# Kernel tuning notes

Hardware: AMD Instinct MI355X
Metric: run time of the kernel (lower is better)

Reference implementation:

```python
import jax, jax.numpy as jnp
import numpy as np

N_NODES = 100000
N_EDGES = 640000
IN_FEATS = 256
HEADS = 4
OUT_FEATS = 32
NEG_SLOPE = 0.2


def setup_inputs() -> dict:
    key = jax.random.key(0)
    k_feat, k_src, k_dst, k_w, k_al, k_ar = jax.random.split(key, 6)
    feat = jax.random.normal(k_feat, (N_NODES, IN_FEATS), dtype=jnp.float32)
    src = jax.random.randint(k_src, (N_EDGES,), 0, N_NODES, dtype=jnp.int32)
    dst = jax.random.randint(k_dst, (N_EDGES,), 0, N_NODES, dtype=jnp.int32)
    # fc: Linear(in_feats, out_feats*num_heads, bias=False); store as [in, H*D]
    W = jax.random.normal(k_w, (IN_FEATS, HEADS * OUT_FEATS), dtype=jnp.float32) * 0.05
    attn_l = jax.random.normal(k_al, (HEADS, OUT_FEATS), dtype=jnp.float32) * 0.1
    attn_r = jax.random.normal(k_ar, (HEADS, OUT_FEATS), dtype=jnp.float32) * 0.1
    return {"feat": feat, "W": W, "attn_l": attn_l, "attn_r": attn_r, "src": src, "dst": dst}


def reference(feat, W, attn_l, attn_r, src, dst):
    N = feat.shape[0]
    H, D = attn_l.shape
    # fc + reshape to [N, H, D]
    ft = (feat @ W).reshape(N, H, D)
    # per-node attention logits [N, H]
    el = jnp.einsum('nhd,hd->nh', ft, attn_l)
    er = jnp.einsum('nhd,hd->nh', ft, attn_r)
    # u_add_v then leaky relu -> per-edge logits [E, H]
    e = el[src] + er[dst]
    e = jnp.where(e > 0, e, NEG_SLOPE * e)
    # edge softmax over incoming edges of each dst node (per head)
    m = jax.ops.segment_max(e, dst, num_segments=N)  # [N, H]
    m = jnp.where(jnp.isfinite(m), m, jnp.zeros_like(m))  # empty segments
    ex = jnp.exp(e - m[dst])
    denom = jax.ops.segment_sum(ex, dst, num_segments=N)  # [N, H]
    a = ex / denom[dst]  # [E, H]
    # u_mul_e + sum aggregation: rst[v] = sum_{(u,v)} a_uv * ft[u]
    msg = ft[src] * a[:, :, None]  # [E, H, D]
    rst = jax.ops.segment_sum(msg, dst, num_segments=N)  # [N, H, D]
    return rst, a[:, :, None]
```

## Files before the change

kernel.cpp:

```cpp
#include <hip/hip_runtime.h>
#include <hip/hip_bf16.h>

#define N_NODES 100000
#define N_EDGES 640000
#define IN_F 256
#define HD 128

using f32x4 = __attribute__((ext_vector_type(4))) float;
using s8v   = __attribute__((ext_vector_type(8))) short;

__device__ __forceinline__ short bf16h(float x) {
  __hip_bfloat16 h = __float2bfloat16(x);
  return (short)__builtin_bit_cast(unsigned short, h);
}
__device__ __forceinline__ float bf16tof(short h) {
  unsigned u = ((unsigned)(unsigned short)h) << 16;
  return __builtin_bit_cast(float, u);
}

__global__ __launch_bounds__(256) void prep_b(const float* __restrict__ W,
                                              short* __restrict__ Bth)
{
  int c = blockIdx.x;
  int k = threadIdx.x;
  Bth[(size_t)c * IN_F + k] = bf16h(W[(size_t)k * HD + c]);
}

__global__ __launch_bounds__(256) void prep_x(const float* __restrict__ W,
    const float* __restrict__ al, const float* __restrict__ ar,
    short* __restrict__ Bxh)
{
  int c = blockIdx.x;
  int k = threadIdx.x;
  float v = 0.f;
  if (c < 8) {
    int h = c & 3;
    const float* att = (c < 4) ? al : ar;
    #pragma unroll
    for (int d = 0; d < 32; d++)
      v += W[(size_t)k * HD + h * 32 + d] * att[h * 32 + d];
  }
  Bxh[(size_t)c * IN_F + k] = bf16h(v);
}

__global__ __launch_bounds__(256) void gemm_mfma(const float* __restrict__ feat,
    const short* __restrict__ Bth, const short* __restrict__ Bxh,
    float* __restrict__ ft, float* __restrict__ el, float* __restrict__ er, int M)
{
  const int wid  = threadIdx.x >> 6;
  const int lane = threadIdx.x & 63;
  const int lr = lane & 15;
  const int lg = lane >> 4;
  const int wm = (wid >> 1) * 32;
  const int wn = (wid & 1) * 64;
  const int rb = blockIdx.x * 64;
  const bool doX = (wid & 1) == 0;

  f32x4 acc[2][4];
  f32x4 accx[2];
  #pragma unroll
  for (int mi = 0; mi < 2; mi++) {
    accx[mi] = (f32x4){0.f, 0.f, 0.f, 0.f};
    #pragma unroll
    for (int ni = 0; ni < 4; ni++) acc[mi][ni] = (f32x4){0.f, 0.f, 0.f, 0.f};
  }

  const float* ap[2];
  #pragma unroll
  for (int mi = 0; mi < 2; mi++) {
    int r = rb + wm + mi * 16 + lr;
    if (r > M - 1) r = M - 1;
    ap[mi] = feat + (size_t)r * IN_F + lg * 8;
  }
  const short* bp[4];
  #pragma unroll
  for (int ni = 0; ni < 4; ni++)
    bp[ni] = Bth + (size_t)(wn + ni * 16 + lr) * IN_F + lg * 8;
  const short* xp = Bxh + (size_t)lr * IN_F + lg * 8;

  float4 A0[3][2], A1[3][2];
  s8v Bb[2][4], Xb[2];

  #pragma unroll
  for (int mi = 0; mi < 2; mi++) {
    A0[0][mi] = *(const float4*)(ap[mi]);       A1[0][mi] = *(const float4*)(ap[mi] + 4);
    A0[1][mi] = *(const float4*)(ap[mi] + 32);  A1[1][mi] = *(const float4*)(ap[mi] + 36);
  }
  #pragma unroll
  for (int ni = 0; ni < 4; ni++) Bb[0][ni] = *(const s8v*)(bp[ni]);
  Xb[0] = *(const s8v*)xp;

  #pragma unroll
  for (int kt = 0; kt < 8; ++kt) {
    const int cur = kt % 3, pre = (kt + 2) % 3;
    const int curb = kt & 1, preb = curb ^ 1;
    if (kt + 2 < 8) {
      #pragma unroll
      for (int mi = 0; mi < 2; mi++) {
        A0[pre][mi] = *(const float4*)(ap[mi] + (kt + 2) * 32);
        A1[pre][mi] = *(const float4*)(ap[mi] + (kt + 2) * 32 + 4);
      }
    }
    if (kt + 1 < 8) {
      #pragma unroll
      for (int ni = 0; ni < 4; ni++) Bb[preb][ni] = *(const s8v*)(bp[ni] + (kt + 1) * 32);
      Xb[preb] = *(const s8v*)(xp + (kt + 1) * 32);
    }
    #pragma unroll
    for (int mi = 0; mi < 2; mi++) {
      const float av[8] = {A0[cur][mi].x, A0[cur][mi].y, A0[cur][mi].z, A0[cur][mi].w,
                           A1[cur][mi].x, A1[cur][mi].y, A1[cur][mi].z, A1[cur][mi].w};
      s8v ah, alo;
      #pragma unroll
      for (int j = 0; j < 8; j++) {
        short h = bf16h(av[j]);
        ah[j]  = h;
        alo[j] = bf16h(av[j] - bf16tof(h));
      }
      #pragma unroll
      for (int ni = 0; ni < 4; ni++) {
        acc[mi][ni] = __builtin_amdgcn_mfma_f32_16x16x32_bf16(ah,  Bb[curb][ni], acc[mi][ni], 0, 0, 0);
        acc[mi][ni] = __builtin_amdgcn_mfma_f32_16x16x32_bf16(alo, Bb[curb][ni], acc[mi][ni], 0, 0, 0);
      }
      if (doX) {
        accx[mi] = __builtin_amdgcn_mfma_f32_16x16x32_bf16(ah,  Xb[curb], accx[mi], 0, 0, 0);
        accx[mi] = __builtin_amdgcn_mfma_f32_16x16x32_bf16(alo, Xb[curb], accx[mi], 0, 0, 0);
      }
    }
  }

  #pragma unroll
  for (int mi = 0; mi < 2; mi++) {
    int rbase = rb + wm + mi * 16 + lg * 4;
    #pragma unroll
    for (int ni = 0; ni < 4; ni++) {
      int col = wn + ni * 16 + lr;
      #pragma unroll
      for (int r = 0; r < 4; r++) {
        int grow = rbase + r;
        if (grow < M) ft[(size_t)grow * HD + col] = acc[mi][ni][r];
      }
    }
    if (doX) {
      #pragma unroll
      for (int r = 0; r < 4; r++) {
        int grow = rbase + r;
        if (grow < M) {
          if (lr < 4)      el[(size_t)grow * 4 + lr]       = accx[mi][r];
          else if (lr < 8) er[(size_t)grow * 4 + (lr - 4)] = accx[mi][r];
        }
      }
    }
  }
}

__global__ void deg_kernel(const int* __restrict__ dst, int* __restrict__ deg) {
  int i = blockIdx.x * blockDim.x + threadIdx.x;
  if (i < N_EDGES) atomicAdd(&deg[dst[i]], 1);
}

__global__ __launch_bounds__(256) void scanA(const int* __restrict__ deg,
    int* __restrict__ excl, int* __restrict__ partials, int n)
{
  __shared__ int s[256];
  int t = threadIdx.x;
  int base = blockIdx.x * 1024 + t * 4;
  int d0 = (base + 0 < n) ? deg[base + 0] : 0;
  int d1 = (base + 1 < n) ? deg[base + 1] : 0;
  int d2 = (base + 2 < n) ? deg[base + 2] : 0;
  int d3 = (base + 3 < n) ? deg[base + 3] : 0;
  int sum = d0 + d1 + d2 + d3;
  s[t] = sum; __syncthreads();
  for (int off = 1; off < 256; off <<= 1) {
    int x = 0; if (t >= off) x = s[t - off];
    __syncthreads(); s[t] += x; __syncthreads();
  }
  int e0 = s[t] - sum;
  if (base + 0 < n) excl[base + 0] = e0;
  if (base + 1 < n) excl[base + 1] = e0 + d0;
  if (base + 2 < n) excl[base + 2] = e0 + d0 + d1;
  if (base + 3 < n) excl[base + 3] = e0 + d0 + d1 + d2;
  if (t == 255) partials[blockIdx.x] = s[255];
}

__global__ void scanB(int* partials, int nb) {
  __shared__ int s[128];
  int t = threadIdx.x;
  int v = (t < nb) ? partials[t] : 0;
  s[t] = v; __syncthreads();
  for (int off = 1; off < 128; off <<= 1) {
    int x = 0; if (t >= off) x = s[t - off];
    __syncthreads(); s[t] += x; __syncthreads();
  }
  if (t < nb) partials[t] = s[t] - v;
}

__global__ __launch_bounds__(256) void scanC(int* __restrict__ row_ptr,
    const int* __restrict__ partials, int n, int E)
{
  int t = threadIdx.x;
  int base = blockIdx.x * 1024 + t * 4;
  int add = partials[blockIdx.x];
  #pragma unroll
  for (int j = 0; j < 4; j++) if (base + j < n) row_ptr[base + j] += add;
  if (blockIdx.x == 0 && t == 0) row_ptr[n] = E;
}

__global__ void scatter_kernel(const int* __restrict__ src, const int* __restrict__ dst,
                               const int* __restrict__ row_ptr,
                               int* __restrict__ cursor, int* __restrict__ usrc) {
  int e = blockIdx.x * blockDim.x + threadIdx.x;
  if (e >= N_EDGES) return;
  int d = dst[e];
  int pos = row_ptr[d] + atomicAdd(&cursor[d], 1);
  usrc[pos] = src[e];
}

__global__ __launch_bounds__(256) void gat_node(const int* __restrict__ row_ptr,
    const int* __restrict__ usrc,
    const float* __restrict__ el, const float* __restrict__ er4,
    const float* __restrict__ ft, float* __restrict__ rst,
    float* __restrict__ lse, int n)
{
  __shared__ int   su[4][64];
  __shared__ float sex[4][64][4];
  const int w = threadIdx.x >> 6;
  const int lane = threadIdx.x & 63;
  const int v = blockIdx.x * 4 + w;
  if (v >= n) return;
  const int s0 = row_ptr[v];
  const int d  = row_ptr[v + 1] - s0;
  const int g  = lane >> 4;

  if (d == 0) {
    *(float2*)(rst + (size_t)v * HD + 2 * lane) = make_float2(0.f, 0.f);
    return;
  }

  const float4 erv = *(const float4*)(er4 + (size_t)v * 4);
  float m0 = -1e30f, m1 = -1e30f, m2 = -1e30f, m3 = -1e30f;
  float den = 0.f;
  float2 acc = make_float2(0.f, 0.f);

  for (int c0 = 0; c0 < d; c0 += 64) {
    const int cd = min(64, d - c0);
    float x0 = -1e30f, x1 = -1e30f, x2 = -1e30f, x3 = -1e30f;
    int u = 0;
    if (lane < cd) {
      u = usrc[s0 + c0 + lane];
      const float4 elv = *(const float4*)(el + (size_t)u * 4);
      x0 = elv.x + erv.x; x0 = x0 > 0.f ? x0 : 0.2f * x0;
      x1 = elv.y + erv.y; x1 = x1 > 0.f ? x1 : 0.2f * x1;
      x2 = elv.z + erv.z; x2 = x2 > 0.f ? x2 : 0.2f * x2;
      x3 = elv.w + erv.w; x3 = x3 > 0.f ? x3 : 0.2f * x3;
    }
    su[w][lane] = u;
    float n0 = x0, n1 = x1, n2 = x2, n3 = x3;
    #pragma unroll
    for (int off = 32; off >= 1; off >>= 1) {
      n0 = fmaxf(n0, __shfl_xor(n0, off));
      n1 = fmaxf(n1, __shfl_xor(n1, off));
      n2 = fmaxf(n2, __shfl_xor(n2, off));
      n3 = fmaxf(n3, __shfl_xor(n3, off));
    }
    n0 = fmaxf(n0, m0); n1 = fmaxf(n1, m1); n2 = fmaxf(n2, m2); n3 = fmaxf(n3, m3);
    float e0 = __expf(x0 - n0), e1 = __expf(x1 - n1);
    float e2 = __expf(x2 - n2), e3 = __expf(x3 - n3);
    sex[w][lane][0] = e0; sex[w][lane][1] = e1;
    sex[w][lane][2] = e2; sex[w][lane][3] = e3;
    float mg = g == 0 ? m0 : g == 1 ? m1 : g == 2 ? m2 : m3;
    float ng = g == 0 ? n0 : g == 1 ? n1 : g == 2 ? n2 : n3;
    float scale = __expf(mg - ng);
    den *= scale; acc.x *= scale; acc.y *= scale;
    m0 = n0; m1 = n1; m2 = n2; m3 = n3;
    asm volatile("s_waitcnt lgkmcnt(0)" ::: "memory");
    #pragma unroll 4
    for (int j = 0; j < cd; ++j) {
      int uu = su[w][j];
      float wgt = sex[w][j][g];
      float2 f = *(const float2*)(ft + (size_t)uu * HD + 2 * lane);
      den += wgt;
      acc.x += wgt * f.x; acc.y += wgt * f.y;
    }
  }
  *(float2*)(rst + (size_t)v * HD + 2 * lane) = make_float2(acc.x / den, acc.y / den);
  if ((lane & 15) == 0) {
    float mg = g == 0 ? m0 : g == 1 ? m1 : g == 2 ? m2 : m3;
    lse[(size_t)v * 4 + g] = mg + __logf(den);
  }
}

__global__ void norm_kernel(const int* __restrict__ src, const int* __restrict__ dst,
                            const float* __restrict__ el, const float* __restrict__ er,
                            const float* __restrict__ lse, float* __restrict__ a, int E)
{
  int i = blockIdx.x * blockDim.x + threadIdx.x;
  if (i >= E) return;
  int u = src[i], v = dst[i];
  const float4 elv = *(const float4*)(el + (size_t)u * 4);
  const float4 erv = *(const float4*)(er + (size_t)v * 4);
  const float4 ls  = *(const float4*)(lse + (size_t)v * 4);
  float x0 = elv.x + erv.x; x0 = x0 > 0.f ? x0 : 0.2f * x0;
  float x1 = elv.y + erv.y; x1 = x1 > 0.f ? x1 : 0.2f * x1;
  float x2 = elv.z + erv.z; x2 = x2 > 0.f ? x2 : 0.2f * x2;
  float x3 = elv.w + erv.w; x3 = x3 > 0.f ? x3 : 0.2f * x3;
  float4 o;
  o.x = __expf(x0 - ls.x); o.y = __expf(x1 - ls.y);
  o.z = __expf(x2 - ls.z); o.w = __expf(x3 - ls.w);
  *(float4*)(a + (size_t)i * 4) = o;
}

extern "C" void kernel_launch(void* const* d_in, const int* in_sizes, int n_in,
                              void* d_out, int out_size, void* d_ws, size_t ws_size,
                              hipStream_t stream)
{
  const float* feat = (const float*)d_in[0];
  const float* W    = (const float*)d_in[1];
  const float* al   = (const float*)d_in[2];
  const float* ar   = (const float*)d_in[3];
  const int*   src  = (const int*)d_in[4];
  const int*   dst  = (const int*)d_in[5];
  float* rst   = (float*)d_out;
  float* a_out = rst + (size_t)N_NODES * HD;

  char* w = (char*)d_ws;
  auto alloc = [&](size_t bytes) { char* p = w; w += (bytes + 255) & ~(size_t)255; return p; };
  float* ft      = (float*)alloc((size_t)N_NODES * HD * 4);
  float* el      = (float*)alloc((size_t)N_NODES * 4 * 4);
  float* er      = (float*)alloc((size_t)N_NODES * 4 * 4);
  float* lse     = (float*)alloc((size_t)N_NODES * 4 * 4);
  int*   deg     = (int*)alloc((size_t)N_NODES * 4);
  int*   row_ptr = (int*)alloc(((size_t)N_NODES + 1) * 4);
  int*   cursor  = (int*)alloc((size_t)N_NODES * 4);
  int*   partials= (int*)alloc(1024);
  int*   usrc    = (int*)alloc((size_t)N_EDGES * 4);
  short* Bth     = (short*)alloc((size_t)HD * IN_F * 2);
  short* Bxh     = (short*)alloc((size_t)16 * IN_F * 2);

  hipMemsetAsync(deg, 0, N_NODES * 4, stream);
  hipMemsetAsync(cursor, 0, N_NODES * 4, stream);

  prep_b<<<128, 256, 0, stream>>>(W, Bth);
  prep_x<<<16, 256, 0, stream>>>(W, al, ar, Bxh);
  gemm_mfma<<<(N_NODES + 63) / 64, 256, 0, stream>>>(feat, Bth, Bxh, ft, el, er, N_NODES);
  deg_kernel<<<(N_EDGES + 255) / 256, 256, 0, stream>>>(dst, deg);
  scanA<<<98, 256, 0, stream>>>(deg, row_ptr, partials, N_NODES);
  scanB<<<1, 128, 0, stream>>>(partials, 98);
  scanC<<<98, 256, 0, stream>>>(row_ptr, partials, N_NODES, N_EDGES);
  scatter_kernel<<<(N_EDGES + 255) / 256, 256, 0, stream>>>(src, dst, row_ptr, cursor, usrc);
  gat_node<<<(N_NODES + 3) / 4, 256, 0, stream>>>(row_ptr, usrc, el, er, ft, rst, lse, N_NODES);
  norm_kernel<<<(N_EDGES + 255) / 256, 256, 0, stream>>>(src, dst, el, er, lse, a_out, N_EDGES);
}
```

Before: 364.4 us.

## Stage GEMM tiles through LDS with async global-to-LDS loads and larger M tile

The feature-projection GEMM now stages A, B and attention-projection tiles into double-buffered LDS using global_load_lds direct copies, instead of per-lane register prefetch from global memory. The block M tile grows from 64 to 128 rows so each B fragment is reused across more rows, and the bf16 conversion uses a manual round-to-nearest-even bit trick. This aims to cut redundant global B loads and improve load efficiency, at the cost of about 50KB of LDS per block, which limits occupancy, plus a barrier per k-step.

Result: faster. 351.3 us (-3.6%).

```diff
diff --git a/kernel.cpp b/kernel.cpp
--- a/kernel.cpp
+++ b/kernel.cpp
@@ -5,25 +5,32 @@
 #define N_EDGES 640000
 #define IN_F 256
 #define HD 128
+#define BM 128
 
 using f32x4 = __attribute__((ext_vector_type(4))) float;
 using s8v   = __attribute__((ext_vector_type(8))) short;
 
-__device__ __forceinline__ short bf16h(float x) {
-  __hip_bfloat16 h = __float2bfloat16(x);
-  return (short)__builtin_bit_cast(unsigned short, h);
+__device__ __forceinline__ short bf16rn(float x) {
+  unsigned u = __builtin_bit_cast(unsigned, x);
+  return (short)((u + 0x7FFFu + ((u >> 16) & 1u)) >> 16);
 }
 __device__ __forceinline__ float bf16tof(short h) {
   unsigned u = ((unsigned)(unsigned short)h) << 16;
   return __builtin_bit_cast(float, u);
 }
 
+typedef const __attribute__((address_space(1))) void gvoid;
+typedef __attribute__((address_space(3))) void lvoid;
+__device__ __forceinline__ void gl_lds16(const void* g, char* l) {
+  __builtin_amdgcn_global_load_lds((gvoid*)g, (lvoid*)l, 16, 0, 0);
+}
+
 __global__ __launch_bounds__(256) void prep_b(const float* __restrict__ W,
                                               short* __restrict__ Bth)
 {
   int c = blockIdx.x;
   int k = threadIdx.x;
-  Bth[(size_t)c * IN_F + k] = bf16h(W[(size_t)k * HD + c]);
+  Bth[(size_t)c * IN_F + k] = bf16rn(W[(size_t)k * HD + c]);
 }
 
 __global__ __launch_bounds__(256) void prep_x(const float* __restrict__ W,
@@ -40,97 +47,105 @@
     for (int d = 0; d < 32; d++)
       v += W[(size_t)k * HD + h * 32 + d] * att[h * 32 + d];
   }
-  Bxh[(size_t)c * IN_F + k] = bf16h(v);
+  Bxh[(size_t)c * IN_F + k] = bf16rn(v);
+}
+
+__device__ __forceinline__ void stage_tile(char* lds, int wid, int lane, int kt,
+    const float* feat, const short* Bth, const short* Bxh, int rb, int M)
+{
+  const int k0 = kt * 32;
+  char* Ab = lds + (kt & 1) * 16384;
+  char* Bb = lds + 32768 + (kt & 1) * 8192;
+  char* Xb = lds + 49152 + (kt & 1) * 1024;
+  #pragma unroll
+  for (int s = 0; s < 6; s++) {
+    const int o = wid + s * 4;
+    if (o < 16) {
+      int cp = o * 64 + lane;
+      int r = cp & 127, kg = cp >> 7;
+      int gr = rb + r; if (gr > M - 1) gr = M - 1;
+      gl_lds16(feat + (size_t)gr * IN_F + k0 + kg * 4, Ab + o * 1024);
+    } else {
+      int j = o - 16;
+      int cp = j * 64 + lane;
+      int c = cp & 127, lg = cp >> 7;
+      gl_lds16(Bth + (size_t)c * IN_F + k0 + lg * 8, Bb + j * 1024);
+    }
+  }
+  if (wid == 0) {
+    int c = lane & 15, lg = lane >> 4;
+    gl_lds16(Bxh + (size_t)c * IN_F + k0 + lg * 8, Xb);
+  }
 }
 
 __global__ __launch_bounds__(256) void gemm_mfma(const float* __restrict__ feat,
     const short* __restrict__ Bth, const short* __restrict__ Bxh,
     float* __restrict__ ft, float* __restrict__ el, float* __restrict__ er, int M)
 {
+  __shared__ char lds[51200];
   const int wid  = threadIdx.x >> 6;
   const int lane = threadIdx.x & 63;
   const int lr = lane & 15;
   const int lg = lane >> 4;
-  const int wm = (wid >> 1) * 32;
+  const int wm = (wid >> 1) * 64;
   const int wn = (wid & 1) * 64;
-  const int rb = blockIdx.x * 64;
+  const int rb = blockIdx.x * BM;
   const bool doX = (wid & 1) == 0;
 
-  f32x4 acc[2][4];
-  f32x4 accx[2];
-  #pragma unroll
-  for (int mi = 0; mi < 2; mi++) {
+  f32x4 acc[4][4];
+  f32x4 accx[4];
+  #pragma unroll
+  for (int mi = 0; mi < 4; mi++) {
     accx[mi] = (f32x4){0.f, 0.f, 0.f, 0.f};
     #pragma unroll
     for (int ni = 0; ni < 4; ni++) acc[mi][ni] = (f32x4){0.f, 0.f, 0.f, 0.f};
   }
 
-  const float* ap[2];
-  #pragma unroll
-  for (int mi = 0; mi < 2; mi++) {
-    int r = rb + wm + mi * 16 + lr;
-    if (r > M - 1) r = M - 1;
-    ap[mi] = feat + (size_t)r * IN_F + lg * 8;
-  }
-  const short* bp[4];
-  #pragma unroll
-  for (int ni = 0; ni < 4; ni++)
-    bp[ni] = Bth + (size_t)(wn + ni * 16 + lr) * IN_F + lg * 8;
-  const short* xp = Bxh + (size_t)lr * IN_F + lg * 8;
-
-  float4 A0[3][2], A1[3][2];
-  s8v Bb[2][4], Xb[2];
-
-  #pragma unroll
-  for (int mi = 0; mi < 2; mi++) {
-    A0[0][mi] = *(const float4*)(ap[mi]);       A1[0][mi] = *(const float4*)(ap[mi] + 4);
-    A0[1][mi] = *(const float4*)(ap[mi] + 32);  A1[1][mi] = *(const float4*)(ap[mi] + 36);
-  }
-  #pragma unroll
-  for (int ni = 0; ni < 4; ni++) Bb[0][ni] = *(const s8v*)(bp[ni]);
-  Xb[0] = *(const s8v*)xp;
+  stage_tile(lds, wid, lane, 0, feat, Bth, Bxh, rb, M);
+  __syncthreads();
 
   #pragma unroll
   for (int kt = 0; kt < 8; ++kt) {
-    const int cur = kt % 3, pre = (kt + 2) % 3;
-    const int curb = kt & 1, preb = curb ^ 1;
-    if (kt + 2 < 8) {
-      #pragma unroll
-      for (int mi = 0; mi < 2; mi++) {
-        A0[pre][mi] = *(const float4*)(ap[mi] + (kt + 2) * 32);
-        A1[pre][mi] = *(const float4*)(ap[mi] + (kt + 2) * 32 + 4);
-      }
-    }
-    if (kt + 1 < 8) {
-      #pragma unroll
-      for (int ni = 0; ni < 4; ni++) Bb[preb][ni] = *(const s8v*)(bp[ni] + (kt + 1) * 32);
-      Xb[preb] = *(const s8v*)(xp + (kt + 1) * 32);
-    }
-    #pragma unroll
-    for (int mi = 0; mi < 2; mi++) {
-      const float av[8] = {A0[cur][mi].x, A0[cur][mi].y, A0[cur][mi].z, A0[cur][mi].w,
-                           A1[cur][mi].x, A1[cur][mi].y, A1[cur][mi].z, A1[cur][mi].w};
+    if (kt < 7) stage_tile(lds, wid, lane, kt + 1, feat, Bth, Bxh, rb, M);
+
+    const char* Ab = lds + (kt & 1) * 16384;
+    const char* Bb = lds + 32768 + (kt & 1) * 8192;
+    const char* Xb = lds + 49152 + (kt & 1) * 1024;
+
+    s8v Bf[4];
+    #pragma unroll
+    for (int ni = 0; ni < 4; ni++)
+      Bf[ni] = *(const s8v*)(Bb + (((lg << 7) + wn + ni * 16 + lr) << 4));
+    s8v Xf = *(const s8v*)(Xb + (((lg << 4) + lr) << 4));
+
+    #pragma unroll
+    for (int mi = 0; mi < 4; mi++) {
+      const int row = wm + mi * 16 + lr;
+      const float4 a0 = *(const float4*)(Ab + ((((lg * 2 + 0) << 7) + row) << 4));
+      const float4 a1 = *(const float4*)(Ab + ((((lg * 2 + 1) << 7) + row) << 4));
+      const float av[8] = {a0.x, a0.y, a0.z, a0.w, a1.x, a1.y, a1.z, a1.w};
       s8v ah, alo;
       #pragma unroll
       for (int j = 0; j < 8; j++) {
-        short h = bf16h(av[j]);
+        short h = bf16rn(av[j]);
         ah[j]  = h;
-        alo[j] = bf16h(av[j] - bf16tof(h));
+        alo[j] = bf16rn(av[j] - bf16tof(h));
       }
       #pragma unroll
       for (int ni = 0; ni < 4; ni++) {
-        acc[mi][ni] = __builtin_amdgcn_mfma_f32_16x16x32_bf16(ah,  Bb[curb][ni], acc[mi][ni], 0, 0, 0);
-        acc[mi][ni] = __builtin_amdgcn_mfma_f32_16x16x32_bf16(alo, Bb[curb][ni], acc[mi][ni], 0, 0, 0);
+        acc[mi][ni] = __builtin_amdgcn_mfma_f32_16x16x32_bf16(ah,  Bf[ni], acc[mi][ni], 0, 0, 0);
+        acc[mi][ni] = __builtin_amdgcn_mfma_f32_16x16x32_bf16(alo, Bf[ni], acc[mi][ni], 0, 0, 0);
       }
       if (doX) {
-        accx[mi] = __builtin_amdgcn_mfma_f32_16x16x32_bf16(ah,  Xb[curb], accx[mi], 0, 0, 0);
-        accx[mi] = __builtin_amdgcn_mfma_f32_16x16x32_bf16(alo, Xb[curb], accx[mi], 0, 0, 0);
-      }
-    }
-  }
-
-  #pragma unroll
-  for (int mi = 0; mi < 2; mi++) {
+        accx[mi] = __builtin_amdgcn_mfma_f32_16x16x32_bf16(ah,  Xf, accx[mi], 0, 0, 0);
+        accx[mi] = __builtin_amdgcn_mfma_f32_16x16x32_bf16(alo, Xf, accx[mi], 0, 0, 0);
+      }
+    }
+    __syncthreads();
+  }
+
+  #pragma unroll
+  for (int mi = 0; mi < 4; mi++) {
     int rbase = rb + wm + mi * 16 + lg * 4;
     #pragma unroll
     for (int ni = 0; ni < 4; ni++) {
@@ -342,7 +357,7 @@
 
   prep_b<<<128, 256, 0, stream>>>(W, Bth);
   prep_x<<<16, 256, 0, stream>>>(W, al, ar, Bxh);
-  gemm_mfma<<<(N_NODES + 63) / 64, 256, 0, stream>>>(feat, Bth, Bxh, ft, el, er, N_NODES);
+  gemm_mfma<<<(N_NODES + BM - 1) / BM, 256, 0, stream>>>(feat, Bth, Bxh, ft, el, er, N_NODES);
   deg_kernel<<<(N_EDGES + 255) / 256, 256, 0, stream>>>(dst, deg);
   scanA<<<98, 256, 0, stream>>>(deg, row_ptr, partials, N_NODES);
   scanB<<<1, 128, 0, stream>>>(partials, 98);
```
